# Kernel optimization log

Measured on AMD Instinct MI355X. Metric: run time of the kernel, lower is better.

The kernel has to match this reference:

```python
import jax, jax.numpy as jnp
import numpy as np

N = 5
C = 256
B, H, W = 8, 64, 64


def setup_inputs() -> dict:
    key = jax.random.key(0)
    ks = jax.random.split(key, 9)
    s = 0.05
    return {
        "inputs": jax.random.normal(ks[0], (B, N, C, H, W), dtype=jnp.float32),
        # grouped 1x1 conv: groups = N-1, each group maps C channels -> 1 channel, no bias
        "wgt_w": jax.random.normal(ks[1], (N - 1, C), dtype=jnp.float32) * s,
        # ConvGRU 1x1 gate convs: in = 2*C (cat of input and hidden), out = C, with bias
        "w_r": jax.random.normal(ks[2], (C, 2 * C), dtype=jnp.float32) * s,
        "b_r": jnp.zeros((C,), dtype=jnp.float32),
        "w_u": jax.random.normal(ks[3], (C, 2 * C), dtype=jnp.float32) * s,
        "b_u": jnp.zeros((C,), dtype=jnp.float32),
        "w_o": jax.random.normal(ks[4], (C, 2 * C), dtype=jnp.float32) * s,
        "b_o": jnp.zeros((C,), dtype=jnp.float32),
        "gamma": jax.random.normal(ks[5], (1,), dtype=jnp.float32) * s,
    }


def _conv1x1(x, Wm, bias):
    # x: [b, cin, h, w]; Wm: [cout, cin]
    return jnp.einsum("bchw,oc->bohw", x, Wm) + bias[None, :, None, None]


def reference(inputs, wgt_w, w_r, b_r, w_u, b_u, w_o, b_o, gamma):
    b, n, c, h, w = inputs.shape

    def gru(x, hprev):
        s = jnp.concatenate([x, hprev], axis=1)  # [b, 2c, h, w]
        u = jax.nn.sigmoid(_conv1x1(s, w_u, b_u))
        r = jax.nn.sigmoid(_conv1x1(s, w_r, b_r))
        o = jnp.tanh(_conv1x1(jnp.concatenate([x, hprev * r], axis=1), w_o, b_o))
        return hprev * (1.0 - u) + o * u

    preds = []
    for i in range(n):
        h_t = inputs[:, i]  # [b, c, h, w]
        idx = [j for j in range(n) if j != i]
        h_n = inputs[:, jnp.array(idx)]  # [b, n-1, c, h, w], neighbor-major channel layout
        diff = h_t[:, None] - h_n  # repeat(h_t, n-1) - cat(neighbors)
        # grouped 1x1 conv (groups = n-1, no bias): per-neighbor channel reduction
        wgt = jnp.einsum("bjchw,jc->bjhw", diff, wgt_w)  # [b, n-1, h, w]
        gate = jax.nn.sigmoid(wgt)
        # torch: wgt.unsqueeze(1).repeat(1, c, 1, 1, 1).view(b, c*(n-1), h, w)
        # -> flat channel index = cc*(n-1) + j  (note: differs from x2's j*c + cc layout)
        gate_full = jnp.broadcast_to(gate[:, None], (b, c, n - 1, h, w)).reshape(
            b, c * (n - 1), h, w
        )
        x2 = h_n.reshape(b, (n - 1) * c, h, w)
        msg = x2 * gate_full
        m_t = msg.reshape(b, n - 1, c, h, w).sum(axis=1)  # sum-aggregate over neighbors
        h_new = gru(m_t, h_t)
        preds.append(h_new * gamma + h_t)
    return jnp.stack(preds, axis=1)  # [b, n, c, h, w]
```

## Files before the change

kernel.cpp:

```cpp
#include <hip/hip_runtime.h>

typedef __attribute__((ext_vector_type(8))) short short8;
typedef __attribute__((ext_vector_type(4))) float f32x4;
typedef __attribute__((ext_vector_type(8))) unsigned short us8;
typedef __attribute__((ext_vector_type(4))) unsigned short us4;

__device__ __forceinline__ float sigmoidf_(float x){ return 1.f/(1.f+__expf(-x)); }
__device__ __forceinline__ unsigned short f2bf(float f){
    union{float f; unsigned int u;} x; x.f = f;
    unsigned int r = x.u + 0x7fffu + ((x.u>>16)&1u);
    return (unsigned short)(r>>16);
}
#define GAS(p) ((const __attribute__((address_space(1))) void*)(uintptr_t)(p))
#define LAS(p) ((__attribute__((address_space(3))) void*)(uintptr_t)(p))

__global__ __launch_bounds__(256) void k_sum(const float* __restrict__ inp, float* __restrict__ S){
    int e = blockIdx.x*256 + threadIdx.x;
    int pl = e & 4095;
    int c  = (e >> 12) & 255;
    int b  = e >> 20;
    float s = 0.f;
    #pragma unroll
    for (int n=0;n<5;n++)
        s += inp[(((size_t)((b*5+n)*256+c))<<12) + pl];
    S[e] = s;
}

__global__ __launch_bounds__(256) void k_dots(const float* __restrict__ inp, const float* __restrict__ wgt,
                                              float* __restrict__ D){
    __shared__ float wg[1024];
    for (int s=threadIdx.x; s<1024; s+=256) wg[s] = wgt[s];
    __syncthreads();
    int e = blockIdx.x*256 + threadIdx.x;
    int pl = e & 4095;
    int bn = e >> 12;
    const float* base = inp + (((size_t)bn*256)<<12) + pl;
    float d0=0,d1=0,d2=0,d3=0;
    #pragma unroll 8
    for (int c=0;c<256;c++){
        float v = base[(size_t)c<<12];
        d0 += v*wg[c]; d1 += v*wg[256+c]; d2 += v*wg[512+c]; d3 += v*wg[768+c];
    }
    size_t o = ((size_t)bn*4)<<12;
    D[o+pl]=d0; D[o+4096+pl]=d1; D[o+8192+pl]=d2; D[o+12288+pl]=d3;
}

__global__ __launch_bounds__(256) void k_gate(const float* __restrict__ D, float* __restrict__ G){
    int e = blockIdx.x*256 + threadIdx.x;
    int pl = e & 4095;
    int r  = e >> 12;
    int j  = r & 3;
    int bi = r >> 2;
    int i  = bi % 5;
    int b  = bi / 5;
    int node = (j < i) ? j : (j+1);
    float w = D[(((size_t)((b*5+i)*4+j))<<12)+pl] - D[(((size_t)((b*5+node)*4+j))<<12)+pl];
    G[e] = sigmoidf_(w);
}

__global__ __launch_bounds__(256) void k_wp(const float* __restrict__ w0, const float* __restrict__ w1,
                                            unsigned short* __restrict__ dst, int OCN){
    int tid = blockIdx.x*256 + threadIdx.x;
    int d = tid*4;
    int kk = d & 63;
    int row = d >> 6;
    int oc = row & (OCN-1);
    int kb = row / OCN;
    int k  = kb*64 + kk;
    const float* src = (oc < 256) ? w0 : w1;
    int ocr = (oc < 256) ? oc : oc-256;
    float4 v = *(const float4*)&src[(size_t)ocr*512 + k];
    us4 pk; pk.x=f2bf(v.x); pk.y=f2bf(v.y); pk.z=f2bf(v.z); pk.w=f2bf(v.w);
    *(us4*)&dst[d] = pk;
}

__global__ __launch_bounds__(256) void k_bx(const float* __restrict__ inp, const float* __restrict__ S,
                                            const float* __restrict__ G,
                                            unsigned short* __restrict__ Alo, unsigned short* __restrict__ Ahi,
                                            int i){
    __shared__ unsigned short tm[64][72];
    __shared__ unsigned short th[64][72];
    int t  = threadIdx.x;
    int c0 = (blockIdx.x & 3) << 6;
    int p0 = (blockIdx.x >> 2) << 6;
    int b  = p0 >> 12, pl0 = p0 & 4095;
    #pragma unroll
    for (int q=0;q<4;q++){
        int s  = t + q*256;
        int c  = s >> 4;
        int pc = (s & 15) << 2;
        int cc = c0 + c;
        float4 h4 = *(const float4*)&inp[(((size_t)((b*5+i)*256+cc))<<12) + pl0 + pc];
        float4 s4 = *(const float4*)&S[(((size_t)(b*256+cc))<<12) + pl0 + pc];
        float4 g4 = *(const float4*)&G[(((size_t)((b*5+i)*4+(cc&3)))<<12) + pl0 + pc];
        tm[c][pc+0]=f2bf(g4.x*(s4.x-h4.x)); tm[c][pc+1]=f2bf(g4.y*(s4.y-h4.y));
        tm[c][pc+2]=f2bf(g4.z*(s4.z-h4.z)); tm[c][pc+3]=f2bf(g4.w*(s4.w-h4.w));
        th[c][pc+0]=f2bf(h4.x); th[c][pc+1]=f2bf(h4.y);
        th[c][pc+2]=f2bf(h4.z); th[c][pc+3]=f2bf(h4.w);
    }
    __syncthreads();
    int kb = c0 >> 6;
    #pragma unroll
    for (int q=0;q<2;q++){
        int s    = t + q*256;
        int p    = s >> 3;
        int cseg = (s & 7) << 3;
        size_t dst = ((size_t)kb*32768 + p0 + p)*64 + cseg;
        us8 vm, vh;
        #pragma unroll
        for (int j=0;j<8;j++){ vm[j]=tm[cseg+j][p]; vh[j]=th[cseg+j][p]; }
        *(us8*)&Alo[dst] = vm;
        *(us8*)&Ahi[dst] = vh;
    }
}

template<int EPI>
__global__ __launch_bounds__(256) void k_mm(
        const unsigned short* __restrict__ Alo, const unsigned short* __restrict__ Ahi,
        const unsigned short* __restrict__ Wb,
        const float* __restrict__ inp, const float* __restrict__ b0, const float* __restrict__ b1,
        float* __restrict__ U, unsigned short* __restrict__ A1hi, float* __restrict__ outp,
        const float* __restrict__ gamma_p, int i)
{
    constexpr int OCN = EPI ? 256 : 512;
    __shared__ unsigned short As[128*64];
    __shared__ unsigned short Bs[128*64];
    int t  = threadIdx.x, wv = t>>6, ln = t&63;
    int p0 = blockIdx.x*128, oc0 = blockIdx.y*128;
    int wm = (wv>>1)*64, wn = (wv&1)*64;
    int row = ln & 15, quad = ln >> 4, kq = quad*8;

    f32x4 acc[4][4];
    f32x4 z = {0.f,0.f,0.f,0.f};
    #pragma unroll
    for (int a=0;a<4;a++){
        #pragma unroll
        for (int o=0;o<4;o++) acc[a][o]=z;
    }

    for (int kb=0; kb<8; ++kb){
        const unsigned short* gA = (kb<4) ? (Alo + ((size_t)kb*32768 + p0)*64)
                                          : (Ahi + ((size_t)(kb-4)*32768 + p0)*64);
        const unsigned short* gW = Wb + ((size_t)kb*OCN + oc0)*64;
        #pragma unroll
        for (int q=0;q<4;q++){
            int off = (wv*4+q)*512;
            __builtin_amdgcn_global_load_lds(GAS(gA + off + ln*8), LAS(Bs + off + ln*8), 16, 0, 0);
            __builtin_amdgcn_global_load_lds(GAS(gW + off + ln*8), LAS(As + off + ln*8), 16, 0, 0);
        }
        __syncthreads();
        #pragma unroll
        for (int ks=0; ks<2; ks++){
            short8 a[4], b[4];
            #pragma unroll
            for (int f=0; f<4; f++){
                a[f] = *(const short8*)&As[(wm+f*16+row)*64 + ks*32 + kq];
                b[f] = *(const short8*)&Bs[(wn+f*16+row)*64 + ks*32 + kq];
            }
            #pragma unroll
            for (int fm=0; fm<4; fm++){
                #pragma unroll
                for (int fn=0; fn<4; fn++)
                    acc[fm][fn] = __builtin_amdgcn_mfma_f32_16x16x32_bf16(a[fm], b[fn], acc[fm][fn], 0,0,0);
            }
        }
        __syncthreads();
    }

    float gm = EPI ? gamma_p[0] : 0.f;
    #pragma unroll
    for (int fn=0; fn<4; fn++){
        int p  = p0 + wn + fn*16 + row;
        int b  = p >> 12, pl = p & 4095;
        size_t hb = (((size_t)((b*5+i)*256))<<12) + pl;
        #pragma unroll
        for (int fm=0; fm<4; fm++){
            int ocb = oc0 + wm + fm*16 + quad*4;
            if (EPI==0){
                if (oc0 < 256){
                    #pragma unroll
                    for (int r=0;r<4;r++){
                        int oc = ocb + r;
                        U[(size_t)oc*32768 + p] = sigmoidf_(acc[fm][fn][r] + b0[oc]);
                    }
                } else {
                    int kb2 = ocb - 256;
                    us4 pk;
                    #pragma unroll
                    for (int r=0;r<4;r++){
                        int c = kb2 + r;
                        float rg = sigmoidf_(acc[fm][fn][r] + b1[c]);
                        float h  = inp[hb + ((size_t)c<<12)];
                        pk[r] = f2bf(rg*h);
                    }
                    *(us4*)&A1hi[((size_t)(kb2>>6)*32768 + p)*64 + (kb2&63)] = pk;
                }
            } else {
                #pragma unroll
                for (int r=0;r<4;r++){
                    int oc = ocb + r;
                    float v  = acc[fm][fn][r] + b0[oc];
                    float e2 = __expf(2.f*v);
                    float thv = 1.f - 2.f/(e2+1.f);
                    float u  = U[(size_t)oc*32768 + p];
                    float h  = inp[hb + ((size_t)oc<<12)];
                    float hn = h*(1.f-u) + thv*u;
                    outp[hb + ((size_t)oc<<12)] = hn*gm + h;
                }
            }
        }
    }
}

extern "C" void kernel_launch(void* const* d_in, const int* in_sizes, int n_in,
                              void* d_out, int out_size, void* d_ws, size_t ws_size,
                              hipStream_t stream) {
    const float* inputs = (const float*)d_in[0];
    const float* wgt_w  = (const float*)d_in[1];
    const float* w_r    = (const float*)d_in[2];
    const float* b_r    = (const float*)d_in[3];
    const float* w_u    = (const float*)d_in[4];
    const float* b_u    = (const float*)d_in[5];
    const float* w_o    = (const float*)d_in[6];
    const float* b_o    = (const float*)d_in[7];
    const float* gamma  = (const float*)d_in[8];
    float* out = (float*)d_out;

    float* S = (float*)d_ws;
    float* D = S + 8388608;
    float* G = D + 655360;
    float* U = G + 655360;
    unsigned short* Alo  = (unsigned short*)(U + 8388608);
    unsigned short* Ahi  = Alo + 8388608;
    unsigned short* A1hi = Ahi + 8388608;
    unsigned short* Wc0  = A1hi + 8388608;
    unsigned short* Wc1  = Wc0 + 262144;

    k_sum <<<32768, 256, 0, stream>>>(inputs, S);
    k_dots<<<640,   256, 0, stream>>>(inputs, wgt_w, D);
    k_gate<<<2560,  256, 0, stream>>>(D, G);
    k_wp  <<<256,   256, 0, stream>>>(w_u, w_r, Wc0, 512);
    k_wp  <<<128,   256, 0, stream>>>(w_o, w_o, Wc1, 256);
    for (int i=0;i<5;i++){
        k_bx<<<2048, 256, 0, stream>>>(inputs, S, G, Alo, Ahi, i);
        k_mm<0><<<dim3(256,4), 256, 0, stream>>>(Alo, Ahi, Wc0, inputs, b_u, b_r,
                                                 U, A1hi, nullptr, gamma, i);
        k_mm<1><<<dim3(256,2), 256, 0, stream>>>(Alo, A1hi, Wc1, inputs, b_o, nullptr,
                                                 U, nullptr, out, gamma, i);
    }
}
```

Measured before the change: 863.0 us.

## Batch GRU node steps across grid z and fuse sum/gate into packing kernel

```diff
diff --git a/kernel.cpp b/kernel.cpp
--- a/kernel.cpp
+++ b/kernel.cpp
@@ -4,6 +4,7 @@
 typedef __attribute__((ext_vector_type(4))) float f32x4;
 typedef __attribute__((ext_vector_type(8))) unsigned short us8;
 typedef __attribute__((ext_vector_type(4))) unsigned short us4;
+typedef __attribute__((ext_vector_type(2))) unsigned short us2;
 
 __device__ __forceinline__ float sigmoidf_(float x){ return 1.f/(1.f+__expf(-x)); }
 __device__ __forceinline__ unsigned short f2bf(float f){
@@ -11,20 +12,13 @@
     unsigned int r = x.u + 0x7fffu + ((x.u>>16)&1u);
     return (unsigned short)(r>>16);
 }
+__device__ __forceinline__ float bf2f(unsigned short u){
+    union{unsigned int u; float f;} x; x.u = ((unsigned int)u)<<16; return x.f;
+}
 #define GAS(p) ((const __attribute__((address_space(1))) void*)(uintptr_t)(p))
 #define LAS(p) ((__attribute__((address_space(3))) void*)(uintptr_t)(p))
 
-__global__ __launch_bounds__(256) void k_sum(const float* __restrict__ inp, float* __restrict__ S){
-    int e = blockIdx.x*256 + threadIdx.x;
-    int pl = e & 4095;
-    int c  = (e >> 12) & 255;
-    int b  = e >> 20;
-    float s = 0.f;
-    #pragma unroll
-    for (int n=0;n<5;n++)
-        s += inp[(((size_t)((b*5+n)*256+c))<<12) + pl];
-    S[e] = s;
-}
+#define SLOT 8388608ull
 
 __global__ __launch_bounds__(256) void k_dots(const float* __restrict__ inp, const float* __restrict__ wgt,
                                               float* __restrict__ D){
@@ -45,72 +39,84 @@
     D[o+pl]=d0; D[o+4096+pl]=d1; D[o+8192+pl]=d2; D[o+12288+pl]=d3;
 }
 
-__global__ __launch_bounds__(256) void k_gate(const float* __restrict__ D, float* __restrict__ G){
-    int e = blockIdx.x*256 + threadIdx.x;
-    int pl = e & 4095;
-    int r  = e >> 12;
-    int j  = r & 3;
-    int bi = r >> 2;
-    int i  = bi % 5;
-    int b  = bi / 5;
-    int node = (j < i) ? j : (j+1);
-    float w = D[(((size_t)((b*5+i)*4+j))<<12)+pl] - D[(((size_t)((b*5+node)*4+j))<<12)+pl];
-    G[e] = sigmoidf_(w);
-}
-
-__global__ __launch_bounds__(256) void k_wp(const float* __restrict__ w0, const float* __restrict__ w1,
-                                            unsigned short* __restrict__ dst, int OCN){
-    int tid = blockIdx.x*256 + threadIdx.x;
+__global__ __launch_bounds__(256) void k_wp2(const float* __restrict__ w_u, const float* __restrict__ w_r,
+                                             const float* __restrict__ w_o,
+                                             unsigned short* __restrict__ Wc0, unsigned short* __restrict__ Wc1){
+    int bx = blockIdx.x;
+    const float *s0, *s1; unsigned short* dst; int OCN, tid;
+    if (bx < 256){ tid = bx*256 + threadIdx.x; OCN = 512; s0 = w_u; s1 = w_r; dst = Wc0; }
+    else         { tid = (bx-256)*256 + threadIdx.x; OCN = 256; s0 = w_o; s1 = w_o; dst = Wc1; }
     int d = tid*4;
     int kk = d & 63;
     int row = d >> 6;
     int oc = row & (OCN-1);
     int kb = row / OCN;
     int k  = kb*64 + kk;
-    const float* src = (oc < 256) ? w0 : w1;
+    const float* src = (oc < 256) ? s0 : s1;
     int ocr = (oc < 256) ? oc : oc-256;
     float4 v = *(const float4*)&src[(size_t)ocr*512 + k];
     us4 pk; pk.x=f2bf(v.x); pk.y=f2bf(v.y); pk.z=f2bf(v.z); pk.w=f2bf(v.w);
     *(us4*)&dst[d] = pk;
 }
 
-__global__ __launch_bounds__(256) void k_bx(const float* __restrict__ inp, const float* __restrict__ S,
-                                            const float* __restrict__ G,
-                                            unsigned short* __restrict__ Alo, unsigned short* __restrict__ Ahi,
-                                            int i){
-    __shared__ unsigned short tm[64][72];
-    __shared__ unsigned short th[64][72];
+__global__ __launch_bounds__(256) void k_bxs(const float* __restrict__ inp, const float* __restrict__ D,
+                                             unsigned short* __restrict__ Alo, unsigned short* __restrict__ Ahi,
+                                             int i0, int cnt){
+    __shared__ unsigned short tm[64*34];
+    __shared__ unsigned short th[64*34];
     int t  = threadIdx.x;
     int c0 = (blockIdx.x & 3) << 6;
-    int p0 = (blockIdx.x >> 2) << 6;
+    int pz = blockIdx.x >> 2;
+    int p0 = pz << 5;
     int b  = p0 >> 12, pl0 = p0 & 4095;
-    #pragma unroll
-    for (int q=0;q<4;q++){
-        int s  = t + q*256;
-        int c  = s >> 4;
-        int pc = (s & 15) << 2;
+
+    f32x4 x[5][2], S4[2];
+    #pragma unroll
+    for (int q=0;q<2;q++){
+        int s = t + q*256;
+        int c = s >> 3, pc = (s&7) << 2;
         int cc = c0 + c;
-        float4 h4 = *(const float4*)&inp[(((size_t)((b*5+i)*256+cc))<<12) + pl0 + pc];
-        float4 s4 = *(const float4*)&S[(((size_t)(b*256+cc))<<12) + pl0 + pc];
-        float4 g4 = *(const float4*)&G[(((size_t)((b*5+i)*4+(cc&3)))<<12) + pl0 + pc];
-        tm[c][pc+0]=f2bf(g4.x*(s4.x-h4.x)); tm[c][pc+1]=f2bf(g4.y*(s4.y-h4.y));
-        tm[c][pc+2]=f2bf(g4.z*(s4.z-h4.z)); tm[c][pc+3]=f2bf(g4.w*(s4.w-h4.w));
-        th[c][pc+0]=f2bf(h4.x); th[c][pc+1]=f2bf(h4.y);
-        th[c][pc+2]=f2bf(h4.z); th[c][pc+3]=f2bf(h4.w);
-    }
-    __syncthreads();
+        f32x4 acc = {0.f,0.f,0.f,0.f};
+        #pragma unroll
+        for (int n=0;n<5;n++){
+            x[n][q] = *(const f32x4*)&inp[(((size_t)((b*5+n)*256+cc))<<12) + pl0 + pc];
+            acc += x[n][q];
+        }
+        S4[q] = acc;
+    }
     int kb = c0 >> 6;
     #pragma unroll
-    for (int q=0;q<2;q++){
-        int s    = t + q*256;
-        int p    = s >> 3;
-        int cseg = (s & 7) << 3;
-        size_t dst = ((size_t)kb*32768 + p0 + p)*64 + cseg;
-        us8 vm, vh;
-        #pragma unroll
-        for (int j=0;j<8;j++){ vm[j]=tm[cseg+j][p]; vh[j]=th[cseg+j][p]; }
-        *(us8*)&Alo[dst] = vm;
-        *(us8*)&Ahi[dst] = vh;
+    for (int i=0;i<5;i++){
+        if (i < i0 || i >= i0+cnt) continue;
+        #pragma unroll
+        for (int q=0;q<2;q++){
+            int s = t + q*256;
+            int c = s >> 3, pc = (s&7) << 2;
+            int j = c & 3;
+            int node = (j < i) ? j : (j+1);
+            f32x4 dw = *(const f32x4*)&D[(((size_t)((b*5+i)*4+j))<<12) + pl0 + pc];
+            f32x4 dn = *(const f32x4*)&D[(((size_t)((b*5+node)*4+j))<<12) + pl0 + pc];
+            f32x4 xi = x[i][q];
+            f32x4 md = S4[q] - xi;
+            int lb = c*34 + pc;
+            us2 m0, m1, h0, h1;
+            m0.x = f2bf(sigmoidf_(dw.x-dn.x)*md.x); m0.y = f2bf(sigmoidf_(dw.y-dn.y)*md.y);
+            m1.x = f2bf(sigmoidf_(dw.z-dn.z)*md.z); m1.y = f2bf(sigmoidf_(dw.w-dn.w)*md.w);
+            h0.x = f2bf(xi.x); h0.y = f2bf(xi.y); h1.x = f2bf(xi.z); h1.y = f2bf(xi.w);
+            *(us2*)&tm[lb] = m0; *(us2*)&tm[lb+2] = m1;
+            *(us2*)&th[lb] = h0; *(us2*)&th[lb+2] = h1;
+        }
+        __syncthreads();
+        {
+            int p = t >> 3, cs = (t&7) << 3;
+            us8 vm, vh;
+            #pragma unroll
+            for (int j8=0;j8<8;j8++){ vm[j8] = tm[(cs+j8)*34 + p]; vh[j8] = th[(cs+j8)*34 + p]; }
+            size_t dst = (size_t)(i - i0)*SLOT + ((size_t)kb*32768 + p0 + p)*64 + cs;
+            *(us8*)&Alo[dst] = vm;
+            *(us8*)&Ahi[dst] = vh;
+        }
+        __syncthreads();
     }
 }
 
@@ -119,28 +125,30 @@
         const unsigned short* __restrict__ Alo, const unsigned short* __restrict__ Ahi,
         const unsigned short* __restrict__ Wb,
         const float* __restrict__ inp, const float* __restrict__ b0, const float* __restrict__ b1,
-        float* __restrict__ U, unsigned short* __restrict__ A1hi, float* __restrict__ outp,
-        const float* __restrict__ gamma_p, int i)
+        unsigned short* __restrict__ U, unsigned short* __restrict__ A1hi, float* __restrict__ outp,
+        const float* __restrict__ gamma_p, int i0)
 {
     constexpr int OCN = EPI ? 256 : 512;
     __shared__ unsigned short As[128*64];
     __shared__ unsigned short Bs[128*64];
     int t  = threadIdx.x, wv = t>>6, ln = t&63;
     int p0 = blockIdx.x*128, oc0 = blockIdx.y*128;
+    int z  = blockIdx.z, i = i0 + z;
+    size_t zo = (size_t)z*SLOT;
     int wm = (wv>>1)*64, wn = (wv&1)*64;
     int row = ln & 15, quad = ln >> 4, kq = quad*8;
 
     f32x4 acc[4][4];
-    f32x4 z = {0.f,0.f,0.f,0.f};
+    f32x4 zr = {0.f,0.f,0.f,0.f};
     #pragma unroll
     for (int a=0;a<4;a++){
         #pragma unroll
-        for (int o=0;o<4;o++) acc[a][o]=z;
+        for (int o=0;o<4;o++) acc[a][o]=zr;
     }
 
     for (int kb=0; kb<8; ++kb){
-        const unsigned short* gA = (kb<4) ? (Alo + ((size_t)kb*32768 + p0)*64)
-                                          : (Ahi + ((size_t)(kb-4)*32768 + p0)*64);
+        const unsigned short* gA = (kb<4) ? (Alo + zo + ((size_t)kb*32768 + p0)*64)
+                                          : (Ahi + zo + ((size_t)(kb-4)*32768 + p0)*64);
         const unsigned short* gW = Wb + ((size_t)kb*OCN + oc0)*64;
         #pragma unroll
         for (int q=0;q<4;q++){
@@ -181,19 +189,19 @@
                     #pragma unroll
                     for (int r=0;r<4;r++){
                         int oc = ocb + r;
-                        U[(size_t)oc*32768 + p] = sigmoidf_(acc[fm][fn][r] + b0[oc]);
+                        U[zo + (size_t)oc*32768 + p] = f2bf(sigmoidf_(acc[fm][fn][r] + b0[oc]));
                     }
                 } else {
                     int kb2 = ocb - 256;
+                    size_t aidx = zo + ((size_t)(kb2>>6)*32768 + p)*64 + (kb2&63);
+                    us4 vh = *(const us4*)&Ahi[aidx];
                     us4 pk;
                     #pragma unroll
                     for (int r=0;r<4;r++){
-                        int c = kb2 + r;
-                        float rg = sigmoidf_(acc[fm][fn][r] + b1[c]);
-                        float h  = inp[hb + ((size_t)c<<12)];
-                        pk[r] = f2bf(rg*h);
+                        float rg = sigmoidf_(acc[fm][fn][r] + b1[kb2+r]);
+                        pk[r] = f2bf(rg * bf2f(vh[r]));
                     }
-                    *(us4*)&A1hi[((size_t)(kb2>>6)*32768 + p)*64 + (kb2&63)] = pk;
+                    *(us4*)&A1hi[aidx] = pk;
                 }
             } else {
                 #pragma unroll
@@ -202,7 +210,7 @@
                     float v  = acc[fm][fn][r] + b0[oc];
                     float e2 = __expf(2.f*v);
                     float thv = 1.f - 2.f/(e2+1.f);
-                    float u  = U[(size_t)oc*32768 + p];
+                    float u  = bf2f(U[zo + (size_t)oc*32768 + p]);
                     float h  = inp[hb + ((size_t)oc<<12)];
                     float hn = h*(1.f-u) + thv*u;
                     outp[hb + ((size_t)oc<<12)] = hn*gm + h;
@@ -226,26 +234,28 @@
     const float* gamma  = (const float*)d_in[8];
     float* out = (float*)d_out;
 
-    float* S = (float*)d_ws;
-    float* D = S + 8388608;
-    float* G = D + 655360;
-    float* U = G + 655360;
-    unsigned short* Alo  = (unsigned short*)(U + 8388608);
-    unsigned short* Ahi  = Alo + 8388608;
-    unsigned short* A1hi = Ahi + 8388608;
-    unsigned short* Wc0  = A1hi + 8388608;
-    unsigned short* Wc1  = Wc0 + 262144;
-
-    k_sum <<<32768, 256, 0, stream>>>(inputs, S);
-    k_dots<<<640,   256, 0, stream>>>(inputs, wgt_w, D);
-    k_gate<<<2560,  256, 0, stream>>>(D, G);
-    k_wp  <<<256,   256, 0, stream>>>(w_u, w_r, Wc0, 512);
-    k_wp  <<<128,   256, 0, stream>>>(w_o, w_o, Wc1, 256);
-    for (int i=0;i<5;i++){
-        k_bx<<<2048, 256, 0, stream>>>(inputs, S, G, Alo, Ahi, i);
-        k_mm<0><<<dim3(256,4), 256, 0, stream>>>(Alo, Ahi, Wc0, inputs, b_u, b_r,
-                                                 U, A1hi, nullptr, gamma, i);
-        k_mm<1><<<dim3(256,2), 256, 0, stream>>>(Alo, A1hi, Wc1, inputs, b_o, nullptr,
-                                                 U, nullptr, out, gamma, i);
-    }
-}
+    float* D = (float*)d_ws;
+    unsigned short* Wc0 = (unsigned short*)(D + 655360);
+    unsigned short* Wc1 = Wc0 + 262144;
+    unsigned short* U   = Wc1 + 131072;
+
+    size_t fixedB = 655360ull*4 + (262144ull + 131072ull)*2;
+    size_t slotB  = 4ull*SLOT*2;
+    int nb = 1;
+    for (int k2=5;k2>=1;k2--){ if (fixedB + (size_t)k2*slotB <= ws_size){ nb = k2; break; } }
+
+    unsigned short* Alo  = U   + (size_t)nb*SLOT;
+    unsigned short* Ahi  = Alo + (size_t)nb*SLOT;
+    unsigned short* A1hi = Ahi + (size_t)nb*SLOT;
+
+    k_dots<<<640, 256, 0, stream>>>(inputs, wgt_w, D);
+    k_wp2 <<<384, 256, 0, stream>>>(w_u, w_r, w_o, Wc0, Wc1);
+    for (int i0=0; i0<5; i0+=nb){
+        int cnt = (5-i0 < nb) ? (5-i0) : nb;
+        k_bxs<<<4096, 256, 0, stream>>>(inputs, D, Alo, Ahi, i0, cnt);
+        k_mm<0><<<dim3(256,4,cnt), 256, 0, stream>>>(Alo, Ahi, Wc0, inputs, b_u, b_r,
+                                                     U, A1hi, nullptr, gamma, i0);
+        k_mm<1><<<dim3(256,2,cnt), 256, 0, stream>>>(Alo, A1hi, Wc1, inputs, b_o, nullptr,
+                                                     U, nullptr, out, gamma, i0);
+    }
+}
```

Result: no change. 872.9 us (+1.1%).
